# Performance work log

Measured on AMD Instinct MI355X. Metric: run time of the kernel, lower is better.

## Reference

```python
import jax, jax.numpy as jnp
import numpy as np

N, E, D, H, G, C = 50000, 600000, 128, 128, 512, 1000
HP = H // 5  # attention-MLP bottleneck (hidden_dim // 5)


def setup_inputs() -> dict:
    key = jax.random.key(0)
    ks = jax.random.split(key, 18)
    cfg_nodes = jax.random.normal(ks[0], (N, D), jnp.float32)
    cfg_relations = jax.random.randint(ks[1], (2, E), 0, N, dtype=jnp.int32)
    pos = jnp.sort(jax.random.randint(ks[2], (G + 1,), 0, N, dtype=jnp.int32))
    node_pos = pos.at[0].set(0).at[-1].set(N)

    def lin(k, fi, fo):
        return jax.random.normal(k, (fi, fo), jnp.float32) / np.sqrt(fi)

    return dict(
        cfg_nodes=cfg_nodes, cfg_relations=cfg_relations, node_pos=node_pos,
        # GATConv layer 1 (in=D, out=H, heads=1)
        W_g1=lin(ks[3], D, H),
        att_src1=jax.random.normal(ks[4], (H,), jnp.float32) / np.sqrt(H),
        att_dst1=jax.random.normal(ks[5], (H,), jnp.float32) / np.sqrt(H),
        b_g1=jnp.zeros((H,), jnp.float32),
        # GATConv layer 2 (in=H, out=H, heads=1, concat=False)
        W_g2=lin(ks[6], H, H),
        att_src2=jax.random.normal(ks[7], (H,), jnp.float32) / np.sqrt(H),
        att_dst2=jax.random.normal(ks[8], (H,), jnp.float32) / np.sqrt(H),
        b_g2=jnp.zeros((H,), jnp.float32),
        # GraphLocalAttention projection MLP
        Wp1=lin(ks[9], H, HP), bp1=jnp.zeros((HP,), jnp.float32),
        Wp2=jax.random.normal(ks[10], (HP,), jnp.float32) / np.sqrt(HP),
        bp2=jnp.zeros((), jnp.float32),
        # final classifier
        Wl=lin(ks[11], H, C), bl=jnp.zeros((C,), jnp.float32),
    )


def _gat_conv(x, src, dst, W, a_src, a_dst, b, n_nodes):
    # PyG GATConv (heads=1): h = xW; e_ij = LeakyReLU(a_s.h_j + a_d.h_i);
    # alpha = softmax over incoming edges of each target; out_i = sum alpha*h_j + b
    h = x @ W                                    # [N, F]
    as_ = h @ a_src                              # [N]
    ad_ = h @ a_dst                              # [N]
    e = jax.nn.leaky_relu(as_[src] + ad_[dst], 0.2)   # [E]
    m = jax.ops.segment_max(e, dst, num_segments=n_nodes)
    ex = jnp.exp(e - m[dst])
    s = jax.ops.segment_sum(ex, dst, num_segments=n_nodes)
    alpha = ex / s[dst]
    out = jax.ops.segment_sum(alpha[:, None] * h[src], dst, num_segments=n_nodes)
    return out + b


def reference(cfg_nodes, cfg_relations, node_pos,
              W_g1, att_src1, att_dst1, b_g1,
              W_g2, att_src2, att_dst2, b_g2,
              Wp1, bp1, Wp2, bp2, Wl, bl):
    n = cfg_nodes.shape[0]
    # add self-loops (PyG GATConv default)
    loops = jnp.arange(n, dtype=cfg_relations.dtype)
    src = jnp.concatenate([cfg_relations[0], loops])
    dst = jnp.concatenate([cfg_relations[1], loops])
    # dropout layers are identity in eval mode
    x = _gat_conv(cfg_nodes, src, dst, W_g1, att_src1, att_dst1, b_g1, n)
    x = jax.nn.elu(x)
    x = _gat_conv(x, src, dst, W_g2, att_src2, att_dst2, b_g2, n)
    # ragged segment attention pooling (attn_by_batch, fully vectorized)
    energy = jax.nn.relu(x @ Wp1 + bp1) @ Wp2 + bp2          # [N]
    seg = jnp.clip(jnp.searchsorted(node_pos, jnp.arange(n), side='right') - 1, 0, G - 1)
    m = jax.ops.segment_max(energy, seg, num_segments=G)
    ex = jnp.exp(energy - m[seg])
    s = jax.ops.segment_sum(ex, seg, num_segments=G)
    w = ex / s[seg]                                           # per-segment softmax
    pooled = jax.ops.segment_sum(w[:, None] * x, seg, num_segments=G)  # [G, H]
    return pooled @ Wl + bl                                   # [G, C]
```

## Files before the change

kernel.cpp:

```cpp
#include <hip/hip_runtime.h>
#include <hip/hip_bf16.h>
#include <math.h>

#define WAVE 64
#define GR 32

typedef __attribute__((ext_vector_type(8))) _Float16 half8;
typedef __attribute__((ext_vector_type(4))) float f32x4;
typedef __attribute__((ext_vector_type(4))) _Float16 half4;

__global__ void count_pack(const int* __restrict__ dst, int* __restrict__ deg, int E, int nbC,
                           const float* __restrict__ W1, const float* __restrict__ W2,
                           _Float16* __restrict__ W1h, _Float16* __restrict__ W2h,
                           const float* __restrict__ Wp1, int HP,
                           _Float16* __restrict__ Ph) {
    int b = blockIdx.x;
    if (b < nbC) {
        int e = (b * 256 + threadIdx.x) * 2;
        if (e + 1 < E) {
            int2 d = *(const int2*)(dst + e);
            atomicAdd(&deg[d.x], 1);
            atomicAdd(&deg[d.y], 1);
        } else if (e < E) {
            atomicAdd(&deg[dst[e]], 1);
        }
    } else if (b < nbC + 128) {
        int pb = b - nbC;
        const float* W = (pb >= 64) ? W2 : W1;
        _Float16* Hf = (pb >= 64) ? W2h : W1h;
        int idx = (pb & 63) * 256 + threadIdx.x;
        int j = idx & 7;
        int lane = (idx >> 3) & 63;
        int kc = (idx >> 9) & 3;
        int nt = idx >> 11;
        int k = kc * 32 + (lane >> 4) * 8 + j;
        int ncol = nt * 16 + (lane & 15);
        Hf[idx] = (_Float16)W[k * 128 + ncol];
    } else {
        int idx = (b - nbC - 128) * 256 + threadIdx.x;
        int j = idx & 7;
        int lane = (idx >> 3) & 63;
        int kc = (idx >> 9) & 3;
        int nt = idx >> 11;
        int k = kc * 32 + (lane >> 4) * 8 + j;
        int ncol = nt * 16 + (lane & 15);
        float x = (ncol < HP) ? Wp1[k * HP + ncol] : 0.f;
        Ph[idx] = (_Float16)x;
    }
}

__global__ void pack_wl(const float* __restrict__ Wl, int C, _Float16* __restrict__ Wlh) {
    int idx = blockIdx.x * 256 + threadIdx.x;
    int j = idx & 7;
    int lane = (idx >> 3) & 63;
    int kc = (idx >> 9) & 3;
    int nt = idx >> 11;
    int k = kc * 32 + (lane >> 4) * 8 + j;
    int ncol = nt * 16 + (lane & 15);
    float x = (ncol < C) ? Wl[(size_t)k * C + ncol] : 0.f;
    Wlh[idx] = (_Float16)x;
}

__global__ void scan_block(const int* __restrict__ in, int* __restrict__ part,
                           int* __restrict__ bsums, int n) {
    __shared__ int tmp[256];
    int tid = threadIdx.x;
    int i = blockIdx.x * 256 + tid;
    int v = (i < n) ? in[i] : 0;
    tmp[tid] = v;
    __syncthreads();
    for (int o = 1; o < 256; o <<= 1) {
        int t = (tid >= o) ? tmp[tid - o] : 0;
        __syncthreads();
        tmp[tid] += t;
        __syncthreads();
    }
    if (i < n) part[i] = tmp[tid] - v;
    if (tid == 255) bsums[blockIdx.x] = tmp[255];
}

__global__ void scan_finish(const int* __restrict__ part, const int* __restrict__ bsums,
                            int* __restrict__ offs, int* __restrict__ cursor,
                            int n, int Etot) {
    __shared__ int acc[256];
    int b = blockIdx.x, tid = threadIdx.x;
    int s = 0;
    for (int i = tid; i < b; i += 256) s += bsums[i];
    acc[tid] = s;
    __syncthreads();
    for (int o = 128; o > 0; o >>= 1) {
        if (tid < o) acc[tid] += acc[tid + o];
        __syncthreads();
    }
    int prefix = acc[0];
    int i = b * 256 + tid;
    if (i < n) {
        int v = part[i] + prefix;
        offs[i] = v;
        cursor[i] = v;
    }
    if (b == 0 && tid == 0) offs[n] = Etot;
}

__global__ void scatter_edges(const int* __restrict__ src, const int* __restrict__ dst,
                              int* __restrict__ cursor, int* __restrict__ csr_src,
                              int* __restrict__ csr_dst, int E) {
    int e = (blockIdx.x * 256 + threadIdx.x) * 2;
    if (e + 1 < E) {
        int2 d = *(const int2*)(dst + e);
        int2 s = *(const int2*)(src + e);
        int p0 = atomicAdd(&cursor[d.x], 1);
        csr_src[p0] = s.x;
        csr_dst[p0] = d.x;
        int p1 = atomicAdd(&cursor[d.y], 1);
        csr_src[p1] = s.y;
        csr_dst[p1] = d.y;
    } else if (e < E) {
        int p = atomicAdd(&cursor[dst[e]], 1);
        csr_src[p] = src[e];
        csr_dst[p] = dst[e];
    }
}

__global__ __launch_bounds__(256) void gemm_mfma(const float* __restrict__ X,
                                                 const _Float16* __restrict__ Bh,
                                                 const float* __restrict__ a_s,
                                                 const float* __restrict__ a_d,
                                                 _Float16* __restrict__ Hout,
                                                 float* __restrict__ as_,
                                                 float* __restrict__ ad_, int n) {
    __shared__ char lds[GR * 136 * 4];
    _Float16* Xh = (_Float16*)lds;
    float* Hs = (float*)lds;

    int tid = threadIdx.x;
    int base = blockIdx.x * GR;
    const float4* X4 = (const float4*)X;

#pragma unroll
    for (int i = 0; i < 4; ++i) {
        int idx = i * 256 + tid;
        int row = idx >> 5, c4 = idx & 31;
        int rs = base + row; if (rs >= n) rs = n - 1;
        float4 v = X4[(size_t)rs * 32 + c4];
        half4 hv = {(_Float16)v.x, (_Float16)v.y, (_Float16)v.z, (_Float16)v.w};
        *(half4*)(Xh + row * 136 + c4 * 4) = hv;
    }
    __syncthreads();

    int wid = tid >> 6, lane = tid & 63;
    int quad = lane >> 4, l16 = lane & 15;
    int rowA = (wid & 1) * 16 + l16;
    int ntb = (wid >> 1) * 4;

    f32x4 acc[4];
#pragma unroll
    for (int t = 0; t < 4; ++t) acc[t] = (f32x4){0.f, 0.f, 0.f, 0.f};

    for (int kc = 0; kc < 4; ++kc) {
        half8 Ah = *(const half8*)(Xh + rowA * 136 + kc * 32 + quad * 8);
#pragma unroll
        for (int nt = 0; nt < 4; ++nt) {
            half8 Bv = *(const half8*)(Bh + (((size_t)((ntb + nt) * 4 + kc)) * 64 + lane) * 8);
            acc[nt] = __builtin_amdgcn_mfma_f32_16x16x32_f16(Ah, Bv, acc[nt], 0, 0, 0);
        }
    }
    __syncthreads();

    int rowD0 = (wid & 1) * 16 + quad * 4;
#pragma unroll
    for (int nt = 0; nt < 4; ++nt)
#pragma unroll
        for (int r = 0; r < 4; ++r)
            Hs[(rowD0 + r) * 136 + (ntb + nt) * 16 + l16] = acc[nt][r];
    __syncthreads();

    const float4* Hs4 = (const float4*)Hs;
    half4* H4 = (half4*)Hout;
#pragma unroll
    for (int i = 0; i < 4; ++i) {
        int idx = i * 256 + tid;
        int row = idx >> 5, c4 = idx & 31;
        int grow = base + row;
        if (grow < n) {
            float4 v = Hs4[row * 34 + c4];
            half4 hv = {(_Float16)v.x, (_Float16)v.y, (_Float16)v.z, (_Float16)v.w};
            H4[(size_t)grow * 32 + c4] = hv;
        }
    }

    int drow = tid >> 3, q = tid & 7;
    const float4* as4 = (const float4*)a_s;
    const float4* ad4 = (const float4*)a_d;
    float s = 0.f, d = 0.f;
#pragma unroll
    for (int j = 0; j < 4; ++j) {
        float4 v = Hs4[drow * 34 + q * 4 + j];
        float4 a = as4[q * 4 + j];
        float4 b = ad4[q * 4 + j];
        s += v.x * a.x + v.y * a.y + v.z * a.z + v.w * a.w;
        d += v.x * b.x + v.y * b.y + v.z * b.z + v.w * b.w;
    }
    s += __shfl_xor(s, 1, WAVE); s += __shfl_xor(s, 2, WAVE); s += __shfl_xor(s, 4, WAVE);
    d += __shfl_xor(d, 1, WAVE); d += __shfl_xor(d, 2, WAVE); d += __shfl_xor(d, 4, WAVE);
    if (q == 0 && base + drow < n) {
        as_[base + drow] = s;
        ad_[base + drow] = d;
    }
}

__device__ __forceinline__ float leaky02(float x) { return x > 0.f ? x : 0.2f * x; }

__global__ __launch_bounds__(256) void edge_weights(const int* __restrict__ csr_src,
                                                    const int* __restrict__ csr_dst,
                                                    const float* __restrict__ as_,
                                                    const float* __restrict__ ad_,
                                                    int2* __restrict__ sw, int E) {
    int i = (blockIdx.x * 256 + threadIdx.x) * 4;
    if (i + 3 < E) {
        int4 s = *(const int4*)(csr_src + i);
        int4 d = *(const int4*)(csr_dst + i);
        float wx = __expf(leaky02(as_[s.x] + ad_[d.x]));
        float wy = __expf(leaky02(as_[s.y] + ad_[d.y]));
        float wz = __expf(leaky02(as_[s.z] + ad_[d.z]));
        float ww = __expf(leaky02(as_[s.w] + ad_[d.w]));
        int4 lo = make_int4(s.x, __float_as_int(wx), s.y, __float_as_int(wy));
        int4 hi = make_int4(s.z, __float_as_int(wz), s.w, __float_as_int(ww));
        *(int4*)(sw + i) = lo;
        *(int4*)(sw + i + 2) = hi;
    } else {
        for (; i < E; ++i) {
            float w = __expf(leaky02(as_[csr_src[i]] + ad_[csr_dst[i]]));
            sw[i] = make_int2(csr_src[i], __float_as_int(w));
        }
    }
}

__global__ __launch_bounds__(256) void gat_aggregate(const _Float16* __restrict__ h,
                                                     const int2* __restrict__ sw,
                                                     const float* __restrict__ as_,
                                                     const float* __restrict__ ad_,
                                                     const int* __restrict__ offs,
                                                     const float* __restrict__ bias,
                                                     float* __restrict__ out, int n, int act) {
    int node = blockIdx.x * 4 + (threadIdx.x >> 6);
    int lane = threadIdx.x & 63;
    if (node >= n) return;
    int beg = offs[node], end = offs[node + 1];
    int q4 = lane >> 4, l = lane & 15;
    const half8* h8 = (const half8*)h;

    float w_self = __expf(leaky02(as_[node] + ad_[node]));
    float facc[8];
    {
        half8 v = h8[(size_t)node * 16 + l];
        float ws = (q4 == 0) ? w_self : 0.f;
#pragma unroll
        for (int i = 0; i < 8; ++i) facc[i] = ws * (float)v[i];
    }
    float sacc = (lane == 0) ? w_self : 0.f;
#pragma unroll 2
    for (int j = beg; j < end; j += 4) {
        int j0 = j + q4;
        bool valid = j0 < end;
        int jc = valid ? j0 : (end - 1);
        int2 e = sw[jc];
        int s = valid ? e.x : node;
        float w = valid ? __int_as_float(e.y) : 0.f;
        half8 v = h8[(size_t)s * 16 + l];
#pragma unroll
        for (int i = 0; i < 8; ++i) facc[i] = fmaf(w, (float)v[i], facc[i]);
        sacc += (l == 0) ? w : 0.f;
    }
#pragma unroll
    for (int i = 0; i < 8; ++i) {
        facc[i] += __shfl_xor(facc[i], 16, WAVE);
        facc[i] += __shfl_xor(facc[i], 32, WAVE);
    }
    sacc += __shfl_xor(sacc, 16, WAVE);
    sacc += __shfl_xor(sacc, 32, WAVE);
    float inv_s = 1.f / __shfl(sacc, 0, WAVE);
    if (q4 == 0) {
        const float4* b4 = (const float4*)bias;
        float4 b0 = b4[l * 2], b1 = b4[l * 2 + 1];
        float4 o0, o1;
        o0.x = fmaf(facc[0], inv_s, b0.x);
        o0.y = fmaf(facc[1], inv_s, b0.y);
        o0.z = fmaf(facc[2], inv_s, b0.z);
        o0.w = fmaf(facc[3], inv_s, b0.w);
        o1.x = fmaf(facc[4], inv_s, b1.x);
        o1.y = fmaf(facc[5], inv_s, b1.y);
        o1.z = fmaf(facc[6], inv_s, b1.z);
        o1.w = fmaf(facc[7], inv_s, b1.w);
        if (act == 1) {
            o0.x = o0.x > 0.f ? o0.x : expm1f(o0.x);
            o0.y = o0.y > 0.f ? o0.y : expm1f(o0.y);
            o0.z = o0.z > 0.f ? o0.z : expm1f(o0.z);
            o0.w = o0.w > 0.f ? o0.w : expm1f(o0.w);
            o1.x = o1.x > 0.f ? o1.x : expm1f(o1.x);
            o1.y = o1.y > 0.f ? o1.y : expm1f(o1.y);
            o1.z = o1.z > 0.f ? o1.z : expm1f(o1.z);
            o1.w = o1.w > 0.f ? o1.w : expm1f(o1.w);
        }
        float4* o4 = (float4*)(out + (size_t)node * 128);
        o4[l * 2] = o0;
        o4[l * 2 + 1] = o1;
    }
}

__global__ __launch_bounds__(256) void energy_mfma(const float* __restrict__ X,
                                                   const _Float16* __restrict__ Ph,
                                                   const float* __restrict__ bp1,
                                                   const float* __restrict__ Wp2,
                                                   const float* __restrict__ bp2,
                                                   float* __restrict__ energy, int n, int HP) {
    __shared__ _Float16 Xh[GR * 136];
    int tid = threadIdx.x;
    int base = blockIdx.x * GR;
    const float4* X4 = (const float4*)X;
#pragma unroll
    for (int i = 0; i < 4; ++i) {
        int idx = i * 256 + tid;
        int row = idx >> 5, c4 = idx & 31;
        int rs = base + row; if (rs >= n) rs = n - 1;
        float4 v = X4[(size_t)rs * 32 + c4];
        half4 hv = {(_Float16)v.x, (_Float16)v.y, (_Float16)v.z, (_Float16)v.w};
        *(half4*)(Xh + row * 136 + c4 * 4) = hv;
    }
    __syncthreads();

    int wid = tid >> 6, lane = tid & 63;
    if (wid >= 2) return;
    int quad = lane >> 4, l16 = lane & 15;
    int rowA = wid * 16 + l16;

    f32x4 acc0 = (f32x4){0.f, 0.f, 0.f, 0.f};
    f32x4 acc1 = (f32x4){0.f, 0.f, 0.f, 0.f};
    for (int kc = 0; kc < 4; ++kc) {
        half8 Ah = *(const half8*)(Xh + rowA * 136 + kc * 32 + quad * 8);
        half8 B0 = *(const half8*)(Ph + (((size_t)kc) * 64 + lane) * 8);
        half8 B1 = *(const half8*)(Ph + (((size_t)(4 + kc)) * 64 + lane) * 8);
        acc0 = __builtin_amdgcn_mfma_f32_16x16x32_f16(Ah, B0, acc0, 0, 0, 0);
        acc1 = __builtin_amdgcn_mfma_f32_16x16x32_f16(Ah, B1, acc1, 0, 0, 0);
    }

    float b0 = bp1[l16];
    float w0 = Wp2[l16];
    int c1 = 16 + l16;
    int c1c = c1 < HP ? c1 : HP - 1;
    float b1 = bp1[c1c];
    float w1 = (c1 < HP) ? Wp2[c1c] : 0.f;
    float bp2v = bp2[0];
#pragma unroll
    for (int r = 0; r < 4; ++r) {
        float h0 = acc0[r] + b0;
        h0 = h0 > 0.f ? h0 : 0.f;
        float h1 = acc1[r] + b1;
        h1 = h1 > 0.f ? h1 : 0.f;
        float v = h0 * w0 + h1 * w1;
        v += __shfl_xor(v, 1, WAVE);
        v += __shfl_xor(v, 2, WAVE);
        v += __shfl_xor(v, 4, WAVE);
        v += __shfl_xor(v, 8, WAVE);
        int row = base + wid * 16 + quad * 4 + r;
        if (l16 == 0 && row < n) energy[row] = v + bp2v;
    }
}

__global__ __launch_bounds__(256) void seg_pool(const float* __restrict__ X,
                                                const float* __restrict__ energy,
                                                const int* __restrict__ node_pos,
                                                float* __restrict__ pooled) {
    int g = blockIdx.x;
    int beg = node_pos[g], end = node_pos[g + 1];
    int tid = threadIdx.x;
    int wid = tid >> 6, lane = tid & 63;
    __shared__ float swr[8];
    __shared__ float4 red[256];

    float m = -INFINITY;
    for (int i = beg + tid; i < end; i += 256) m = fmaxf(m, energy[i]);
#pragma unroll
    for (int o = 1; o < 64; o <<= 1) m = fmaxf(m, __shfl_xor(m, o, WAVE));
    if (lane == 0) swr[wid] = m;
    __syncthreads();
    m = fmaxf(fmaxf(swr[0], swr[1]), fmaxf(swr[2], swr[3]));

    float s = 0.f;
    for (int i = beg + tid; i < end; i += 256) s += __expf(energy[i] - m);
#pragma unroll
    for (int o = 1; o < 64; o <<= 1) s += __shfl_xor(s, o, WAVE);
    if (lane == 0) swr[4 + wid] = s;
    __syncthreads();
    s = swr[4] + swr[5] + swr[6] + swr[7];
    float inv = (end > beg && s > 0.f) ? 1.f / s : 0.f;

    int quad = tid & 31;
    int rg = tid >> 5;
    const float4* X4 = (const float4*)X;
    float4 acc = make_float4(0.f, 0.f, 0.f, 0.f);
#pragma unroll 2
    for (int i = beg + rg; i < end; i += 8) {
        float w = __expf(energy[i] - m) * inv;
        float4 v = X4[(size_t)i * 32 + quad];
        acc.x = fmaf(w, v.x, acc.x);
        acc.y = fmaf(w, v.y, acc.y);
        acc.z = fmaf(w, v.z, acc.z);
        acc.w = fmaf(w, v.w, acc.w);
    }
    red[tid] = acc;
    __syncthreads();
    if (rg < 4) {
        float4 o = red[tid + 128];
        acc.x += o.x; acc.y += o.y; acc.z += o.z; acc.w += o.w;
        red[tid] = acc;
    }
    __syncthreads();
    if (rg < 2) {
        float4 o = red[tid + 64];
        acc.x += o.x; acc.y += o.y; acc.z += o.z; acc.w += o.w;
        red[tid] = acc;
    }
    __syncthreads();
    if (rg == 0) {
        float4 o = red[tid + 32];
        acc.x += o.x; acc.y += o.y; acc.z += o.z; acc.w += o.w;
        ((float4*)(pooled + (size_t)g * 128))[quad] = acc;
    }
}

__global__ __launch_bounds__(256) void classify_mfma(const float* __restrict__ P,
                                                     const _Float16* __restrict__ Wlh,
                                                     const float* __restrict__ bl,
                                                     float* __restrict__ out,
                                                     int G_, int C, int nbM) {
    __shared__ _Float16 Xh[GR * 136];
    int tid = threadIdx.x;
    int bm = blockIdx.x % nbM;
    int bn = blockIdx.x / nbM;
    int base = bm * GR;
    const float4* X4 = (const float4*)P;
#pragma unroll
    for (int i = 0; i < 4; ++i) {
        int idx = i * 256 + tid;
        int row = idx >> 5, c4 = idx & 31;
        int rs = base + row; if (rs >= G_) rs = G_ - 1;
        float4 v = X4[(size_t)rs * 32 + c4];
        half4 hv = {(_Float16)v.x, (_Float16)v.y, (_Float16)v.z, (_Float16)v.w};
        *(half4*)(Xh + row * 136 + c4 * 4) = hv;
    }
    __syncthreads();

    int wid = tid >> 6, lane = tid & 63;
    int quad = lane >> 4, l16 = lane & 15;
    int rowA = (wid & 1) * 16 + l16;
    int ntb = bn * 8 + (wid >> 1) * 4;

    f32x4 acc[4];
#pragma unroll
    for (int t = 0; t < 4; ++t) acc[t] = (f32x4){0.f, 0.f, 0.f, 0.f};

    for (int kc = 0; kc < 4; ++kc) {
        half8 Ah = *(const half8*)(Xh + rowA * 136 + kc * 32 + quad * 8);
#pragma unroll
        for (int nt = 0; nt < 4; ++nt) {
            half8 Bv = *(const half8*)(Wlh + (((size_t)((ntb + nt) * 4 + kc)) * 64 + lane) * 8);
            acc[nt] = __builtin_amdgcn_mfma_f32_16x16x32_f16(Ah, Bv, acc[nt], 0, 0, 0);
        }
    }

    int row0 = base + (wid & 1) * 16 + quad * 4;
#pragma unroll
    for (int nt = 0; nt < 4; ++nt) {
        int col = (ntb + nt) * 16 + l16;
        if (col < C) {
            float b = bl[col];
#pragma unroll
            for (int r = 0; r < 4; ++r) {
                int row = row0 + r;
                if (row < G_) out[(size_t)row * C + col] = acc[nt][r] + b;
            }
        }
    }
}

extern "C" void kernel_launch(void* const* d_in, const int* in_sizes, int n_in,
                              void* d_out, int out_size, void* d_ws, size_t ws_size,
                              hipStream_t stream) {
    const float* cfg_nodes = (const float*)d_in[0];
    const int* rel = (const int*)d_in[1];
    const int* node_pos = (const int*)d_in[2];
    const float* W_g1 = (const float*)d_in[3];
    const float* att_src1 = (const float*)d_in[4];
    const float* att_dst1 = (const float*)d_in[5];
    const float* b_g1 = (const float*)d_in[6];
    const float* W_g2 = (const float*)d_in[7];
    const float* att_src2 = (const float*)d_in[8];
    const float* att_dst2 = (const float*)d_in[9];
    const float* b_g2 = (const float*)d_in[10];
    const float* Wp1 = (const float*)d_in[11];
    const float* bp1 = (const float*)d_in[12];
    const float* Wp2 = (const float*)d_in[13];
    const float* bp2 = (const float*)d_in[14];
    const float* Wl = (const float*)d_in[15];
    const float* bl = (const float*)d_in[16];

    const int N = in_sizes[0] / 128;
    const int E = in_sizes[1] / 2;
    const int G = in_sizes[2] - 1;
    const int HP = in_sizes[12];
    const int C = out_size / G;

    const int* srcArr = rel;
    const int* dstArr = rel + E;

    char* w = (char*)d_ws;
    auto carve = [&](size_t bytes) -> char* {
        char* p = w;
        w += (bytes + 255) & ~(size_t)255;
        return p;
    };
    _Float16* bufH = (_Float16*)carve((size_t)N * 128 * 2);
    float* bufB = (float*)carve((size_t)N * 128 * 4);
    float* asv = (float*)carve((size_t)N * 4);
    float* adv = (float*)carve((size_t)N * 4);
    float* energy = (float*)carve((size_t)N * 4);
    int* deg = (int*)carve((size_t)N * 4);
    int* offs = (int*)carve((size_t)(N + 1) * 4);
    int* cursor = (int*)carve((size_t)N * 4);
    int* csr_src = (int*)carve((size_t)E * 4);
    int* csr_dst = (int*)carve((size_t)E * 4);
    int2* swbuf = (int2*)carve((size_t)E * 8);
    int* bsums = (int*)carve(1024);
    _Float16* W1h = (_Float16*)carve(16384 * 2);
    _Float16* W2h = (_Float16*)carve(16384 * 2);
    _Float16* Ph = (_Float16*)carve(4096 * 2);
    _Float16* Wlh = (_Float16*)carve(131072 * 2);
    float* pooled = (float*)carve((size_t)G * 128 * 4);

    const int nbN = (N + 255) / 256;
    const int nbC = ((E + 1) / 2 + 255) / 256;
    const int nbT = (N + GR - 1) / GR;
    const int nbW = (E + 1023) / 1024;
    const int nbM = (G + GR - 1) / GR;
    const int nbCt = (C + 127) / 128;

    hipMemsetAsync(deg, 0, (size_t)N * 4, stream);
    count_pack<<<nbC + 144, 256, 0, stream>>>(dstArr, deg, E, nbC,
                                              W_g1, W_g2, W1h, W2h, Wp1, HP, Ph);
    pack_wl<<<512, 256, 0, stream>>>(Wl, C, Wlh);
    scan_block<<<nbN, 256, 0, stream>>>(deg, offs, bsums, N);
    scan_finish<<<nbN, 256, 0, stream>>>(offs, bsums, offs, cursor, N, E);
    scatter_edges<<<nbC, 256, 0, stream>>>(srcArr, dstArr, cursor, csr_src, csr_dst, E);

    gemm_mfma<<<nbT, 256, 0, stream>>>(cfg_nodes, W1h, att_src1, att_dst1,
                                       bufH, asv, adv, N);
    edge_weights<<<nbW, 256, 0, stream>>>(csr_src, csr_dst, asv, adv, swbuf, E);
    gat_aggregate<<<(N + 3) / 4, 256, 0, stream>>>(bufH, swbuf, asv, adv, offs, b_g1, bufB, N, 1);

    gemm_mfma<<<nbT, 256, 0, stream>>>(bufB, W2h, att_src2, att_dst2,
                                       bufH, asv, adv, N);
    edge_weights<<<nbW, 256, 0, stream>>>(csr_src, csr_dst, asv, adv, swbuf, E);
    gat_aggregate<<<(N + 3) / 4, 256, 0, stream>>>(bufH, swbuf, asv, adv, offs, b_g2, bufB, N, 0);

    energy_mfma<<<nbT, 256, 0, stream>>>(bufB, Ph, bp1, Wp2, bp2, energy, N, HP);
    seg_pool<<<G, 256, 0, stream>>>(bufB, energy, node_pos, pooled);
    classify_mfma<<<nbM * nbCt, 256, 0, stream>>>(pooled, Wlh, bl, (float*)d_out, G, C, nbM);
}
```

Before: 304.8 us.

## Store GAT aggregate outputs as fp16 and split segment pooling across column halves

The intermediate node features written by gat_aggregate are now fp16 instead of fp32. Every consumer (the second-layer GEMM via a new fp16-input variant, the energy MLP, and segment pooling) reads them as fp16, which halves the traffic for a 25.6 MB buffer. Segment pooling now launches two blocks per graph, each covering 64 columns with 16 row groups. This adds parallelism, and the reduction loop is generalized to match. Features are rounded to fp16 one step earlier, which slightly changes numerics.

After: 301.1 us. No clear change (-1.2%).

```diff
diff --git a/kernel.cpp b/kernel.cpp
--- a/kernel.cpp
+++ b/kernel.cpp
@@ -209,6 +209,91 @@
     }
 }
 
+__global__ __launch_bounds__(256) void gemm_mfma_h(const _Float16* __restrict__ X,
+                                                   const _Float16* __restrict__ Bh,
+                                                   const float* __restrict__ a_s,
+                                                   const float* __restrict__ a_d,
+                                                   _Float16* __restrict__ Hout,
+                                                   float* __restrict__ as_,
+                                                   float* __restrict__ ad_, int n) {
+    __shared__ char lds[GR * 136 * 4];
+    _Float16* Xh = (_Float16*)lds;
+    float* Hs = (float*)lds;
+
+    int tid = threadIdx.x;
+    int base = blockIdx.x * GR;
+    const half8* X8 = (const half8*)X;
+
+#pragma unroll
+    for (int i = 0; i < 2; ++i) {
+        int idx = i * 256 + tid;
+        int row = idx >> 4, c8 = idx & 15;
+        int rs = base + row; if (rs >= n) rs = n - 1;
+        *(half8*)(Xh + row * 136 + c8 * 8) = X8[(size_t)rs * 16 + c8];
+    }
+    __syncthreads();
+
+    int wid = tid >> 6, lane = tid & 63;
+    int quad = lane >> 4, l16 = lane & 15;
+    int rowA = (wid & 1) * 16 + l16;
+    int ntb = (wid >> 1) * 4;
+
+    f32x4 acc[4];
+#pragma unroll
+    for (int t = 0; t < 4; ++t) acc[t] = (f32x4){0.f, 0.f, 0.f, 0.f};
+
+    for (int kc = 0; kc < 4; ++kc) {
+        half8 Ah = *(const half8*)(Xh + rowA * 136 + kc * 32 + quad * 8);
+#pragma unroll
+        for (int nt = 0; nt < 4; ++nt) {
+            half8 Bv = *(const half8*)(Bh + (((size_t)((ntb + nt) * 4 + kc)) * 64 + lane) * 8);
+            acc[nt] = __builtin_amdgcn_mfma_f32_16x16x32_f16(Ah, Bv, acc[nt], 0, 0, 0);
+        }
+    }
+    __syncthreads();
+
+    int rowD0 = (wid & 1) * 16 + quad * 4;
+#pragma unroll
+    for (int nt = 0; nt < 4; ++nt)
+#pragma unroll
+        for (int r = 0; r < 4; ++r)
+            Hs[(rowD0 + r) * 136 + (ntb + nt) * 16 + l16] = acc[nt][r];
+    __syncthreads();
+
+    const float4* Hs4 = (const float4*)Hs;
+    half4* H4 = (half4*)Hout;
+#pragma unroll
+    for (int i = 0; i < 4; ++i) {
+        int idx = i * 256 + tid;
+        int row = idx >> 5, c4 = idx & 31;
+        int grow = base + row;
+        if (grow < n) {
+            float4 v = Hs4[row * 34 + c4];
+            half4 hv = {(_Float16)v.x, (_Float16)v.y, (_Float16)v.z, (_Float16)v.w};
+            H4[(size_t)grow * 32 + c4] = hv;
+        }
+    }
+
+    int drow = tid >> 3, q = tid & 7;
+    const float4* as4 = (const float4*)a_s;
+    const float4* ad4 = (const float4*)a_d;
+    float s = 0.f, d = 0.f;
+#pragma unroll
+    for (int j = 0; j < 4; ++j) {
+        float4 v = Hs4[drow * 34 + q * 4 + j];
+        float4 a = as4[q * 4 + j];
+        float4 b = ad4[q * 4 + j];
+        s += v.x * a.x + v.y * a.y + v.z * a.z + v.w * a.w;
+        d += v.x * b.x + v.y * b.y + v.z * b.z + v.w * b.w;
+    }
+    s += __shfl_xor(s, 1, WAVE); s += __shfl_xor(s, 2, WAVE); s += __shfl_xor(s, 4, WAVE);
+    d += __shfl_xor(d, 1, WAVE); d += __shfl_xor(d, 2, WAVE); d += __shfl_xor(d, 4, WAVE);
+    if (q == 0 && base + drow < n) {
+        as_[base + drow] = s;
+        ad_[base + drow] = d;
+    }
+}
+
 __device__ __forceinline__ float leaky02(float x) { return x > 0.f ? x : 0.2f * x; }
 
 __global__ __launch_bounds__(256) void edge_weights(const int* __restrict__ csr_src,
@@ -242,7 +327,7 @@
                                                      const float* __restrict__ ad_,
                                                      const int* __restrict__ offs,
                                                      const float* __restrict__ bias,
-                                                     float* __restrict__ out, int n, int act) {
+                                                     _Float16* __restrict__ out, int n, int act) {
     int node = blockIdx.x * 4 + (threadIdx.x >> 6);
     int lane = threadIdx.x & 63;
     if (node >= n) return;
@@ -283,32 +368,27 @@
     if (q4 == 0) {
         const float4* b4 = (const float4*)bias;
         float4 b0 = b4[l * 2], b1 = b4[l * 2 + 1];
-        float4 o0, o1;
-        o0.x = fmaf(facc[0], inv_s, b0.x);
-        o0.y = fmaf(facc[1], inv_s, b0.y);
-        o0.z = fmaf(facc[2], inv_s, b0.z);
-        o0.w = fmaf(facc[3], inv_s, b0.w);
-        o1.x = fmaf(facc[4], inv_s, b1.x);
-        o1.y = fmaf(facc[5], inv_s, b1.y);
-        o1.z = fmaf(facc[6], inv_s, b1.z);
-        o1.w = fmaf(facc[7], inv_s, b1.w);
+        float o[8];
+        o[0] = fmaf(facc[0], inv_s, b0.x);
+        o[1] = fmaf(facc[1], inv_s, b0.y);
+        o[2] = fmaf(facc[2], inv_s, b0.z);
+        o[3] = fmaf(facc[3], inv_s, b0.w);
+        o[4] = fmaf(facc[4], inv_s, b1.x);
+        o[5] = fmaf(facc[5], inv_s, b1.y);
+        o[6] = fmaf(facc[6], inv_s, b1.z);
+        o[7] = fmaf(facc[7], inv_s, b1.w);
         if (act == 1) {
-            o0.x = o0.x > 0.f ? o0.x : expm1f(o0.x);
-            o0.y = o0.y > 0.f ? o0.y : expm1f(o0.y);
-            o0.z = o0.z > 0.f ? o0.z : expm1f(o0.z);
-            o0.w = o0.w > 0.f ? o0.w : expm1f(o0.w);
-            o1.x = o1.x > 0.f ? o1.x : expm1f(o1.x);
-            o1.y = o1.y > 0.f ? o1.y : expm1f(o1.y);
-            o1.z = o1.z > 0.f ? o1.z : expm1f(o1.z);
-            o1.w = o1.w > 0.f ? o1.w : expm1f(o1.w);
-        }
-        float4* o4 = (float4*)(out + (size_t)node * 128);
-        o4[l * 2] = o0;
-        o4[l * 2 + 1] = o1;
-    }
-}
-
-__global__ __launch_bounds__(256) void energy_mfma(const float* __restrict__ X,
+#pragma unroll
+            for (int i = 0; i < 8; ++i) o[i] = o[i] > 0.f ? o[i] : expm1f(o[i]);
+        }
+        half8 hv;
+#pragma unroll
+        for (int i = 0; i < 8; ++i) hv[i] = (_Float16)o[i];
+        ((half8*)(out + (size_t)node * 128))[l] = hv;
+    }
+}
+
+__global__ __launch_bounds__(256) void energy_mfma(const _Float16* __restrict__ X,
                                                    const _Float16* __restrict__ Ph,
                                                    const float* __restrict__ bp1,
                                                    const float* __restrict__ Wp2,
@@ -317,15 +397,13 @@
     __shared__ _Float16 Xh[GR * 136];
     int tid = threadIdx.x;
     int base = blockIdx.x * GR;
-    const float4* X4 = (const float4*)X;
-#pragma unroll
-    for (int i = 0; i < 4; ++i) {
+    const half8* X8 = (const half8*)X;
+#pragma unroll
+    for (int i = 0; i < 2; ++i) {
         int idx = i * 256 + tid;
-        int row = idx >> 5, c4 = idx & 31;
+        int row = idx >> 4, c8 = idx & 15;
         int rs = base + row; if (rs >= n) rs = n - 1;
-        float4 v = X4[(size_t)rs * 32 + c4];
-        half4 hv = {(_Float16)v.x, (_Float16)v.y, (_Float16)v.z, (_Float16)v.w};
-        *(half4*)(Xh + row * 136 + c4 * 4) = hv;
+        *(half8*)(Xh + row * 136 + c8 * 8) = X8[(size_t)rs * 16 + c8];
     }
     __syncthreads();
 
@@ -367,11 +445,12 @@
     }
 }
 
-__global__ __launch_bounds__(256) void seg_pool(const float* __restrict__ X,
+__global__ __launch_bounds__(256) void seg_pool(const _Float16* __restrict__ X,
                                                 const float* __restrict__ energy,
                                                 const int* __restrict__ node_pos,
                                                 float* __restrict__ pooled) {
-    int g = blockIdx.x;
+    int g = blockIdx.x >> 1;
+    int bn = blockIdx.x & 1;
     int beg = node_pos[g], end = node_pos[g + 1];
     int tid = threadIdx.x;
     int wid = tid >> 6, lane = tid & 63;
@@ -395,38 +474,31 @@
     s = swr[4] + swr[5] + swr[6] + swr[7];
     float inv = (end > beg && s > 0.f) ? 1.f / s : 0.f;
 
-    int quad = tid & 31;
-    int rg = tid >> 5;
-    const float4* X4 = (const float4*)X;
+    int cq = tid & 15;
+    int rg = tid >> 4;
+    const half4* X4 = (const half4*)X;
     float4 acc = make_float4(0.f, 0.f, 0.f, 0.f);
 #pragma unroll 2
-    for (int i = beg + rg; i < end; i += 8) {
+    for (int i = beg + rg; i < end; i += 16) {
         float w = __expf(energy[i] - m) * inv;
-        float4 v = X4[(size_t)i * 32 + quad];
-        acc.x = fmaf(w, v.x, acc.x);
-        acc.y = fmaf(w, v.y, acc.y);
-        acc.z = fmaf(w, v.z, acc.z);
-        acc.w = fmaf(w, v.w, acc.w);
+        half4 v = X4[(size_t)i * 32 + bn * 16 + cq];
+        acc.x = fmaf(w, (float)v.x, acc.x);
+        acc.y = fmaf(w, (float)v.y, acc.y);
+        acc.z = fmaf(w, (float)v.z, acc.z);
+        acc.w = fmaf(w, (float)v.w, acc.w);
     }
     red[tid] = acc;
-    __syncthreads();
-    if (rg < 4) {
-        float4 o = red[tid + 128];
-        acc.x += o.x; acc.y += o.y; acc.z += o.z; acc.w += o.w;
-        red[tid] = acc;
-    }
-    __syncthreads();
-    if (rg < 2) {
-        float4 o = red[tid + 64];
-        acc.x += o.x; acc.y += o.y; acc.z += o.z; acc.w += o.w;
-        red[tid] = acc;
-    }
-    __syncthreads();
-    if (rg == 0) {
-        float4 o = red[tid + 32];
-        acc.x += o.x; acc.y += o.y; acc.z += o.z; acc.w += o.w;
-        ((float4*)(pooled + (size_t)g * 128))[quad] = acc;
-    }
+#pragma unroll
+    for (int o = 8; o >= 1; o >>= 1) {
+        __syncthreads();
+        if (rg < o) {
+            float4 t = red[tid + o * 16];
+            acc.x += t.x; acc.y += t.y; acc.z += t.z; acc.w += t.w;
+            red[tid] = acc;
+        }
+    }
+    if (rg == 0)
+        ((float4*)(pooled + (size_t)g * 128 + bn * 64))[cq] = acc;
 }
 
 __global__ __launch_bounds__(256) void classify_mfma(const float* __restrict__ P,
@@ -521,7 +593,7 @@
         return p;
     };
     _Float16* bufH = (_Float16*)carve((size_t)N * 128 * 2);
-    float* bufB = (float*)carve((size_t)N * 128 * 4);
+    _Float16* bufF = (_Float16*)carve((size_t)N * 128 * 2);
     float* asv = (float*)carve((size_t)N * 4);
     float* adv = (float*)carve((size_t)N * 4);
     float* energy = (float*)carve((size_t)N * 4);
@@ -556,14 +628,14 @@
     gemm_mfma<<<nbT, 256, 0, stream>>>(cfg_nodes, W1h, att_src1, att_dst1,
                                        bufH, asv, adv, N);
     edge_weights<<<nbW, 256, 0, stream>>>(csr_src, csr_dst, asv, adv, swbuf, E);
-    gat_aggregate<<<(N + 3) / 4, 256, 0, stream>>>(bufH, swbuf, asv, adv, offs, b_g1, bufB, N, 1);
-
-    gemm_mfma<<<nbT, 256, 0, stream>>>(bufB, W2h, att_src2, att_dst2,
-                                       bufH, asv, adv, N);
+    gat_aggregate<<<(N + 3) / 4, 256, 0, stream>>>(bufH, swbuf, asv, adv, offs, b_g1, bufF, N, 1);
+
+    gemm_mfma_h<<<nbT, 256, 0, stream>>>(bufF, W2h, att_src2, att_dst2,
+                                         bufH, asv, adv, N);
     edge_weights<<<nbW, 256, 0, stream>>>(csr_src, csr_dst, asv, adv, swbuf, E);
-    gat_aggregate<<<(N + 3) / 4, 256, 0, stream>>>(bufH, swbuf, asv, adv, offs, b_g2, bufB, N, 0);
-
-    energy_mfma<<<nbT, 256, 0, stream>>>(bufB, Ph, bp1, Wp2, bp2, energy, N, HP);
-    seg_pool<<<G, 256, 0, stream>>>(bufB, energy, node_pos, pooled);
+    gat_aggregate<<<(N + 3) / 4, 256, 0, stream>>>(bufH, swbuf, asv, adv, offs, b_g2, bufF, N, 0);
+
+    energy_mfma<<<nbT, 256, 0, stream>>>(bufF, Ph, bp1, Wp2, bp2, energy, N, HP);
+    seg_pool<<<G * 2, 256, 0, stream>>>(bufF, energy, node_pos, pooled);
     classify_mfma<<<nbM * nbCt, 256, 0, stream>>>(pooled, Wlh, bl, (float*)d_out, G, C, nbM);
 }
```
